# Optimization experiments

Measured on AMD Instinct MI355X. Metric: run time of the kernel, lower is better.

## Reference

```python
import jax, jax.numpy as jnp
import numpy as np

D, L, H = 256, 8, 64  # data_dim, latent_dim, hidden_dim (depth=3 hidden layers)


def setup_inputs() -> dict:
    key = jax.random.key(0)
    ks = jax.random.split(key, 9)
    s_in = 1.0 / np.sqrt(L)
    s_h = 1.0 / np.sqrt(H)
    return {
        "z": jax.random.normal(ks[0], (4096, D, L), dtype=jnp.float32),
        # stacked per-coordinate MLP params: layer i weight (D, in, out), bias (D, out)
        "W1": jax.random.uniform(ks[1], (D, L, H), jnp.float32, -s_in, s_in),
        "b1": jax.random.uniform(ks[2], (D, H), jnp.float32, -s_in, s_in),
        "W2": jax.random.uniform(ks[3], (D, H, H), jnp.float32, -s_h, s_h),
        "b2": jax.random.uniform(ks[4], (D, H), jnp.float32, -s_h, s_h),
        "W3": jax.random.uniform(ks[5], (D, H, H), jnp.float32, -s_h, s_h),
        "b3": jax.random.uniform(ks[6], (D, H), jnp.float32, -s_h, s_h),
        "Wo": jax.random.uniform(ks[7], (D, H, 1), jnp.float32, -s_h, s_h),
        "bo": jax.random.uniform(ks[8], (D, 1), jnp.float32, -s_h, s_h),
    }


def reference(z, W1, b1, W2, b2, W3, b3, Wo, bo):
    # Batched grouped MLP: all data_dim per-coordinate nets in one einsum per layer.
    h = jax.nn.silu(jnp.einsum("bdl,dlh->bdh", z, W1) + b1)   # (B, D, H)
    h = jax.nn.silu(jnp.einsum("bdh,dhk->bdk", h, W2) + b2)
    h = jax.nn.silu(jnp.einsum("bdh,dhk->bdk", h, W3) + b3)
    out = jnp.einsum("bdh,dho->bdo", h, Wo) + bo              # (B, D, 1)
    return out[..., 0]                                        # (B, D) == torch.cat(coords, dim=1)
```

## Files before the change

### kernel.cpp

```cpp
#include <hip/hip_runtime.h>
#include <hip/hip_bf16.h>


#define NDIM 256
#define LDIM 8
#define HDIM 64
#define BDIM 4096
#define BT   128

#define REC_W1P   0
#define REC_W2H   3072
#define REC_W2L   11264
#define REC_W3H   19456
#define REC_W3L   27648
#define REC_COEF  35840
#define REC_SIZE  36864

#define ACT_HI    36864
#define ACT_LO    53248
#define OUTBUF    69632
#define LDS_SIZE  70656

typedef __bf16 bf16x8 __attribute__((ext_vector_type(8)));
typedef __bf16 bf16x4 __attribute__((ext_vector_type(4)));
typedef float  f32x4  __attribute__((ext_vector_type(4)));

__device__ __forceinline__ float silu_f(float x) {
  return x * __builtin_amdgcn_rcpf(1.0f + __expf(-x));
}

__global__ void setup_weights(const float* __restrict__ W1, const float* __restrict__ b1,
                              const float* __restrict__ W2, const float* __restrict__ b2,
                              const float* __restrict__ W3, const float* __restrict__ b3,
                              const float* __restrict__ Wo, char* __restrict__ ws) {
  const int d = blockIdx.x;
  const int y = blockIdx.y;
  const int t = threadIdx.x;
  __shared__ float tile[64 * 65];
  char* rec = ws + (size_t)d * REC_SIZE;

  if (y == 0) {
    for (int idx = t; idx < LDIM * HDIM; idx += 256)
      tile[(idx >> 6) * 65 + (idx & 63)] = W1[d * LDIM * HDIM + idx];
    __syncthreads();
    if (t < 64) {
      __bf16* w1p = (__bf16*)(rec + REC_W1P) + t * 24;
#pragma unroll
      for (int ks = 0; ks < 8; ++ks) {
        float f = tile[ks * 65 + t];
        __bf16 h = (__bf16)f;
        w1p[ks] = h;
        w1p[8 + ks] = h;
        w1p[16 + ks] = (__bf16)(f - (float)h);
      }
    }
    float* coef = (float*)(rec + REC_COEF);
    float v;
    if (t < 64)       v = b1[d * 64 + t];
    else if (t < 128) v = b2[d * 64 + (t - 64)];
    else if (t < 192) v = b3[d * 64 + (t - 128)];
    else              v = Wo[d * 64 + (t - 192)];
    coef[t] = v;
  } else {
    const float* src = (y == 1 ? W2 : W3) + (size_t)d * 4096;
    const int hibase = (y == 1 ? REC_W2H : REC_W3H);
    for (int idx = t; idx < 4096; idx += 256)
      tile[(idx >> 6) * 65 + (idx & 63)] = src[idx];
    __syncthreads();
    const int tt = t & 127;
    const bool isLo = (t >= 128);
    const int o = tt >> 1, hh = tt & 1;
    __bf16* dst = (__bf16*)(rec + hibase + (isLo ? 8192 : 0));
#pragma unroll
    for (int cc = 0; cc < 4; ++cc) {
      const int cp = hh * 4 + cc;
      const int kc = cp ^ (o & 7);
#pragma unroll
      for (int j = 0; j < 8; ++j) {
        float f = tile[(kc * 8 + j) * 65 + o];
        __bf16 h = (__bf16)f;
        dst[o * 64 + cp * 8 + j] = isLo ? (__bf16)(f - (float)h) : h;
      }
    }
  }
}

__device__ __forceinline__ void mid_layer(const char* __restrict__ smem, int whbase, int boff,
                                          f32x4 (&acc)[2][4], int wm, int wp, int l15, int lg, int x7) {
  const int co = (lg ^ x7) * 16;
#pragma unroll
  for (int mt = 0; mt < 2; ++mt) {
    f32x4 b = *(const f32x4*)(smem + REC_COEF + boff + wm * 128 + mt * 64 + lg * 16);
#pragma unroll
    for (int nt = 0; nt < 4; ++nt) acc[mt][nt] = b;
  }
  int aw[2], ab[4];
#pragma unroll
  for (int mt = 0; mt < 2; ++mt) aw[mt] = whbase + (wm * 32 + mt * 16 + l15) * 128 + co;
#pragma unroll
  for (int nt = 0; nt < 4; ++nt) ab[nt] = ACT_HI + (wp * 64 + nt * 16 + l15) * 128 + co;

#pragma unroll
  for (int ks = 0; ks < 2; ++ks) {
    const int kx = ks * 64;
    bf16x8 ah[2], al[2], bh[4], bl[4];
#pragma unroll
    for (int mt = 0; mt < 2; ++mt) {
      const char* p = smem + (aw[mt] ^ kx);
      ah[mt] = *(const bf16x8*)p;
      al[mt] = *(const bf16x8*)(p + 8192);
    }
#pragma unroll
    for (int nt = 0; nt < 4; ++nt) {
      const char* p = smem + (ab[nt] ^ kx);
      bh[nt] = *(const bf16x8*)p;
      bl[nt] = *(const bf16x8*)(p + 16384);
    }
#pragma unroll
    for (int mt = 0; mt < 2; ++mt)
#pragma unroll
      for (int nt = 0; nt < 4; ++nt)
        acc[mt][nt] = __builtin_amdgcn_mfma_f32_16x16x32_bf16(ah[mt], bh[nt], acc[mt][nt], 0, 0, 0);
#pragma unroll
    for (int mt = 0; mt < 2; ++mt)
#pragma unroll
      for (int nt = 0; nt < 4; ++nt)
        acc[mt][nt] = __builtin_amdgcn_mfma_f32_16x16x32_bf16(ah[mt], bl[nt], acc[mt][nt], 0, 0, 0);
#pragma unroll
    for (int mt = 0; mt < 2; ++mt)
#pragma unroll
      for (int nt = 0; nt < 4; ++nt)
        acc[mt][nt] = __builtin_amdgcn_mfma_f32_16x16x32_bf16(al[mt], bh[nt], acc[mt][nt], 0, 0, 0);
  }
}

__device__ __forceinline__ void transition(f32x4 (&acc)[2][4], char* __restrict__ smem,
                                           int wm, int wp, int l15, int lg, int x7) {
  const int h8 = (lg & 1) * 8;
#pragma unroll
  for (int mt = 0; mt < 2; ++mt) {
    const int c = wm * 4 + mt * 2 + (lg >> 1);
    const int coff = ((c ^ x7) * 16) + h8;
#pragma unroll
    for (int nt = 0; nt < 4; ++nt) {
      const int r = wp * 64 + nt * 16 + l15;
      bf16x4 hv, lv;
#pragma unroll
      for (int i = 0; i < 4; ++i) {
        float s = silu_f(acc[mt][nt][i]);
        __bf16 h = (__bf16)s;
        hv[i] = h;
        lv[i] = (__bf16)(s - (float)h);
      }
      char* p = smem + ACT_HI + r * 128 + coff;
      *(bf16x4*)p = hv;
      *(bf16x4*)(p + 16384) = lv;
    }
  }
}

__global__ __launch_bounds__(256, 2)
void mlp_main(const float* __restrict__ z, const char* __restrict__ ws,
              const float* __restrict__ bo, float* __restrict__ out) {
  __shared__ __align__(16) char smem[LDS_SIZE];

  const int bx  = (int)blockIdx.x;
  const int swz = (bx & 7) * 1024 + (bx >> 3);
  const int d   = swz >> 5;
  const int b0  = (swz & 31) * BT;

  const int t    = (int)threadIdx.x;
  const int lane = t & 63;
  const int wave = t >> 6;
  const int wm  = wave & 1;
  const int wp  = wave >> 1;
  const int l15 = lane & 15;
  const int lg  = lane >> 4;
  const int x7  = l15 & 7;

  bf16x8 zf[4];
#pragma unroll
  for (int nt = 0; nt < 4; ++nt) {
    const int r = b0 + wp * 64 + nt * 16 + l15;
    const float* zp = z + ((size_t)r * NDIM + d) * LDIM;
    float4 q0 = *(const float4*)zp;
    float4 q1 = *(const float4*)(zp + 4);
    float f[8] = {q0.x, q0.y, q0.z, q0.w, q1.x, q1.y, q1.z, q1.w};
    bf16x8 hv, lv;
#pragma unroll
    for (int j = 0; j < 8; ++j) {
      __bf16 h = (__bf16)f[j];
      hv[j] = h;
      lv[j] = (__bf16)(f[j] - (float)h);
    }
    zf[nt] = (lg & 1) ? lv : hv;
  }

  {
    const float4* gsrc = (const float4*)(ws + (size_t)d * REC_SIZE);
    float4* ldst = (float4*)smem;
    for (int i = t; i < REC_SIZE / 16; i += 256) ldst[i] = gsrc[i];
  }
  __syncthreads();

  f32x4 acc[2][4];

  {
    bf16x8 a1[2];
#pragma unroll
    for (int mt = 0; mt < 2; ++mt) {
      if (lg < 3) {
        a1[mt] = *(const bf16x8*)(smem + REC_W1P + (wm * 32 + mt * 16 + l15) * 48 + lg * 16);
      } else {
        a1[mt] = (bf16x8)((__bf16)0.0f);
      }
    }
#pragma unroll
    for (int mt = 0; mt < 2; ++mt) {
      f32x4 b = *(const f32x4*)(smem + REC_COEF + wm * 128 + mt * 64 + lg * 16);
#pragma unroll
      for (int nt = 0; nt < 4; ++nt) acc[mt][nt] = b;
    }
#pragma unroll
    for (int mt = 0; mt < 2; ++mt)
#pragma unroll
      for (int nt = 0; nt < 4; ++nt)
        acc[mt][nt] = __builtin_amdgcn_mfma_f32_16x16x32_bf16(a1[mt], zf[nt], acc[mt][nt], 0, 0, 0);
  }

  transition(acc, smem, wm, wp, l15, lg, x7);
  __syncthreads();

  mid_layer(smem, REC_W2H, 256, acc, wm, wp, l15, lg, x7);
  __syncthreads();
  transition(acc, smem, wm, wp, l15, lg, x7);
  __syncthreads();

  mid_layer(smem, REC_W3H, 512, acc, wm, wp, l15, lg, x7);

  float* outBuf = (float*)(smem + OUTBUF);
  f32x4 wof[2];
#pragma unroll
  for (int mt = 0; mt < 2; ++mt)
    wof[mt] = *(const f32x4*)(smem + REC_COEF + 768 + wm * 128 + mt * 64 + lg * 16);
#pragma unroll
  for (int nt = 0; nt < 4; ++nt) {
    float part = 0.0f;
#pragma unroll
    for (int mt = 0; mt < 2; ++mt)
#pragma unroll
      for (int i = 0; i < 4; ++i)
        part += silu_f(acc[mt][nt][i]) * wof[mt][i];
    part += __shfl_xor(part, 16);
    part += __shfl_xor(part, 32);
    if (lg == 0) outBuf[wm * 128 + wp * 64 + nt * 16 + l15] = part;
  }
  __syncthreads();
  if (t < BT) out[(size_t)(b0 + t) * NDIM + d] = outBuf[t] + outBuf[128 + t] + bo[d];
}

extern "C" void kernel_launch(void* const* d_in, const int* in_sizes, int n_in,
                              void* d_out, int out_size, void* d_ws, size_t ws_size,
                              hipStream_t stream) {
  const float* z  = (const float*)d_in[0];
  const float* W1 = (const float*)d_in[1];
  const float* b1 = (const float*)d_in[2];
  const float* W2 = (const float*)d_in[3];
  const float* b2 = (const float*)d_in[4];
  const float* W3 = (const float*)d_in[5];
  const float* b3 = (const float*)d_in[6];
  const float* Wo = (const float*)d_in[7];
  const float* bo = (const float*)d_in[8];
  float* out = (float*)d_out;
  char* ws = (char*)d_ws;

  setup_weights<<<dim3(NDIM, 3), 256, 0, stream>>>(W1, b1, W2, b2, W3, b3, Wo, ws);
  mlp_main<<<NDIM * (BDIM / BT), 256, 0, stream>>>(z, ws, bo, out);
}
```

Baseline: 214.6 us.

## Read weight fragments directly from global memory instead of staging in LDS

The main kernel no longer copies the per-coordinate weight record (about 36 KB) into shared memory. MFMA operand fragments and biases are now loaded straight from global memory, and setup_weights writes W2/W3 in a plain, unswizzled layout suited to those direct loads. Shared memory shrinks to the activation buffers, which lets launch bounds request 3 blocks per SIMD for higher occupancy. The trade-off is that every wave refetches weights through L1/L2, giving more global-load latency in the inner MFMA loop and register pressure under the tighter bound.

```diff
diff --git a/kernel.cpp b/kernel.cpp
--- a/kernel.cpp
+++ b/kernel.cpp
@@ -16,10 +16,10 @@
 #define REC_COEF  35840
 #define REC_SIZE  36864
 
-#define ACT_HI    36864
-#define ACT_LO    53248
-#define OUTBUF    69632
-#define LDS_SIZE  70656
+#define ACT_HI    0
+#define ACT_LO    16384
+#define OUTBUF    32768
+#define LDS_SIZE  33792
 
 typedef __bf16 bf16x8 __attribute__((ext_vector_type(8)));
 typedef __bf16 bf16x4 __attribute__((ext_vector_type(4)));
@@ -67,36 +67,40 @@
     for (int idx = t; idx < 4096; idx += 256)
       tile[(idx >> 6) * 65 + (idx & 63)] = src[idx];
     __syncthreads();
-    const int tt = t & 127;
-    const bool isLo = (t >= 128);
-    const int o = tt >> 1, hh = tt & 1;
-    __bf16* dst = (__bf16*)(rec + hibase + (isLo ? 8192 : 0));
-#pragma unroll
-    for (int cc = 0; cc < 4; ++cc) {
-      const int cp = hh * 4 + cc;
-      const int kc = cp ^ (o & 7);
-#pragma unroll
-      for (int j = 0; j < 8; ++j) {
-        float f = tile[(kc * 8 + j) * 65 + o];
-        __bf16 h = (__bf16)f;
-        dst[o * 64 + cp * 8 + j] = isLo ? (__bf16)(f - (float)h) : h;
-      }
-    }
-  }
-}
-
-__device__ __forceinline__ void mid_layer(const char* __restrict__ smem, int whbase, int boff,
-                                          f32x4 (&acc)[2][4], int wm, int wp, int l15, int lg, int x7) {
+    const int o = t >> 2;
+    const int q = t & 3;
+    bf16x8 h0, h1, l0, l1;
+#pragma unroll
+    for (int j = 0; j < 8; ++j) {
+      float f = tile[(q * 16 + j) * 65 + o];
+      __bf16 h = (__bf16)f;
+      h0[j] = h; l0[j] = (__bf16)(f - (float)h);
+      float g = tile[(q * 16 + 8 + j) * 65 + o];
+      __bf16 hg = (__bf16)g;
+      h1[j] = hg; l1[j] = (__bf16)(g - (float)hg);
+    }
+    char* dst = rec + hibase + o * 128 + q * 32;
+    *(bf16x8*)(dst)              = h0;
+    *(bf16x8*)(dst + 16)         = h1;
+    *(bf16x8*)(dst + 8192)       = l0;
+    *(bf16x8*)(dst + 8192 + 16)  = l1;
+  }
+}
+
+__device__ __forceinline__ void mid_layer(const char* __restrict__ wh, const float* __restrict__ biasf,
+                                          const char* __restrict__ smem, f32x4 (&acc)[2][4],
+                                          int wm, int wp, int l15, int lg, int x7) {
   const int co = (lg ^ x7) * 16;
 #pragma unroll
   for (int mt = 0; mt < 2; ++mt) {
-    f32x4 b = *(const f32x4*)(smem + REC_COEF + boff + wm * 128 + mt * 64 + lg * 16);
+    f32x4 b = *(const f32x4*)(biasf + wm * 32 + mt * 16 + lg * 4);
 #pragma unroll
     for (int nt = 0; nt < 4; ++nt) acc[mt][nt] = b;
   }
-  int aw[2], ab[4];
-#pragma unroll
-  for (int mt = 0; mt < 2; ++mt) aw[mt] = whbase + (wm * 32 + mt * 16 + l15) * 128 + co;
+  const char* aw[2];
+  int ab[4];
+#pragma unroll
+  for (int mt = 0; mt < 2; ++mt) aw[mt] = wh + (wm * 32 + mt * 16 + l15) * 128 + lg * 16;
 #pragma unroll
   for (int nt = 0; nt < 4; ++nt) ab[nt] = ACT_HI + (wp * 64 + nt * 16 + l15) * 128 + co;
 
@@ -106,7 +110,7 @@
     bf16x8 ah[2], al[2], bh[4], bl[4];
 #pragma unroll
     for (int mt = 0; mt < 2; ++mt) {
-      const char* p = smem + (aw[mt] ^ kx);
+      const char* p = aw[mt] + kx;
       ah[mt] = *(const bf16x8*)p;
       al[mt] = *(const bf16x8*)(p + 8192);
     }
@@ -159,7 +163,7 @@
   }
 }
 
-__global__ __launch_bounds__(256, 2)
+__global__ __launch_bounds__(256, 3)
 void mlp_main(const float* __restrict__ z, const char* __restrict__ ws,
               const float* __restrict__ bo, float* __restrict__ out) {
   __shared__ __align__(16) char smem[LDS_SIZE];
@@ -178,6 +182,9 @@
   const int lg  = lane >> 4;
   const int x7  = l15 & 7;
 
+  const char* rec   = ws + (size_t)d * REC_SIZE;
+  const float* coef = (const float*)(rec + REC_COEF);
+
   bf16x8 zf[4];
 #pragma unroll
   for (int nt = 0; nt < 4; ++nt) {
@@ -196,13 +203,6 @@
     zf[nt] = (lg & 1) ? lv : hv;
   }
 
-  {
-    const float4* gsrc = (const float4*)(ws + (size_t)d * REC_SIZE);
-    float4* ldst = (float4*)smem;
-    for (int i = t; i < REC_SIZE / 16; i += 256) ldst[i] = gsrc[i];
-  }
-  __syncthreads();
-
   f32x4 acc[2][4];
 
   {
@@ -210,14 +210,14 @@
 #pragma unroll
     for (int mt = 0; mt < 2; ++mt) {
       if (lg < 3) {
-        a1[mt] = *(const bf16x8*)(smem + REC_W1P + (wm * 32 + mt * 16 + l15) * 48 + lg * 16);
+        a1[mt] = *(const bf16x8*)(rec + REC_W1P + (wm * 32 + mt * 16 + l15) * 48 + lg * 16);
       } else {
         a1[mt] = (bf16x8)((__bf16)0.0f);
       }
     }
 #pragma unroll
     for (int mt = 0; mt < 2; ++mt) {
-      f32x4 b = *(const f32x4*)(smem + REC_COEF + wm * 128 + mt * 64 + lg * 16);
+      f32x4 b = *(const f32x4*)(coef + wm * 32 + mt * 16 + lg * 4);
 #pragma unroll
       for (int nt = 0; nt < 4; ++nt) acc[mt][nt] = b;
     }
@@ -231,18 +231,18 @@
   transition(acc, smem, wm, wp, l15, lg, x7);
   __syncthreads();
 
-  mid_layer(smem, REC_W2H, 256, acc, wm, wp, l15, lg, x7);
+  mid_layer(rec + REC_W2H, coef + 64, smem, acc, wm, wp, l15, lg, x7);
   __syncthreads();
   transition(acc, smem, wm, wp, l15, lg, x7);
   __syncthreads();
 
-  mid_layer(smem, REC_W3H, 512, acc, wm, wp, l15, lg, x7);
+  mid_layer(rec + REC_W3H, coef + 128, smem, acc, wm, wp, l15, lg, x7);
 
   float* outBuf = (float*)(smem + OUTBUF);
   f32x4 wof[2];
 #pragma unroll
   for (int mt = 0; mt < 2; ++mt)
-    wof[mt] = *(const f32x4*)(smem + REC_COEF + 768 + wm * 128 + mt * 64 + lg * 16);
+    wof[mt] = *(const f32x4*)(coef + 192 + wm * 32 + mt * 16 + lg * 4);
 #pragma unroll
   for (int nt = 0; nt < 4; ++nt) {
     float part = 0.0f;
```

Result: faster. 208.9 us (-2.7%).
